# Optimization experiments

Measured on AMD Instinct MI355X. Metric: run time of the kernel, lower is better.

The kernel has to match this reference:

```python
import jax, jax.numpy as jnp
import numpy as np

EPS = 1e-5  # BatchNorm eps (torch default)

def _bn(x, mean, var, gamma, beta):
    # eval-mode BatchNorm over the trailing (heads, ch) axes
    return (x - mean) * (gamma / jnp.sqrt(var + EPS)) + beta

def setup_inputs() -> dict:
    key = jax.random.key(0)
    ks = jax.random.split(key, 8)
    B, C, W, H = 16, 256, 64, 64
    heads, k, u, m = 4, 16, 1, 23
    vv = 256
    kh, vh = k // heads, vv // heads
    x = jax.random.normal(ks[0], (B, C, W, H), dtype=jnp.float32)
    q_w = jax.random.normal(ks[1], (heads, kh, C), dtype=jnp.float32) * 0.05
    k_w = jax.random.normal(ks[2], (heads, kh * u, C), dtype=jnp.float32) * 0.05
    v_w = jax.random.normal(ks[3], (heads, vh * u, C), dtype=jnp.float32) * 0.05
    q_gamma = 0.5 + jax.random.uniform(ks[4], (heads, kh), dtype=jnp.float32)
    q_beta = jax.random.normal(ks[5], (heads, kh), dtype=jnp.float32) * 0.1
    q_mean = jnp.zeros((heads, kh), dtype=jnp.float32)
    q_var = jnp.ones((heads, kh), dtype=jnp.float32)
    k_gamma = 0.5 + jax.random.uniform(ks[6], (heads, kh * u), dtype=jnp.float32)
    k_beta = jax.random.normal(ks[7], (heads, kh * u), dtype=jnp.float32) * 0.1
    k_mean = jnp.zeros((heads, kh * u), dtype=jnp.float32)
    k_var = jnp.ones((heads, kh * u), dtype=jnp.float32)
    embedding = jax.random.normal(jax.random.fold_in(key, 99), (kh, heads, u, 1, m, m), dtype=jnp.float32) * 0.05
    return {"x": x, "q_w": q_w, "q_gamma": q_gamma, "q_beta": q_beta, "q_mean": q_mean,
            "q_var": q_var, "k_w": k_w, "k_gamma": k_gamma, "k_beta": k_beta,
            "k_mean": k_mean, "k_var": k_var, "v_w": v_w, "embedding": embedding}

def reference(x, q_w, q_gamma, q_beta, q_mean, q_var, k_w, k_gamma, k_beta, k_mean, k_var, v_w, embedding):
    B, C, W, H = x.shape
    heads, kh, _ = q_w.shape
    u = embedding.shape[2]
    m = embedding.shape[-1]
    vh = v_w.shape[1] // u
    pad = (m - 1) // 2

    # 1x1 conv projections (all heads stacked) -> channels-last
    q = jnp.einsum('bcxy,hkc->bxyhk', x, q_w)                      # [B,W,H,heads,kh]
    q = _bn(q, q_mean, q_var, q_gamma, q_beta)
    kk = jnp.einsum('bcxy,hkc->bxyhk', x, k_w)                     # [B,W,H,heads,kh*u]
    kk = _bn(kk, k_mean, k_var, k_gamma, k_beta)
    # softmax over all spatial positions, per (head, key-channel)
    sm = jax.nn.softmax(kk.reshape(B, W * H, heads, kh * u), axis=1)
    sm = sm.reshape(B, W, H, heads, kh, u)                          # [B,W,H,h,kh,u]
    v = jnp.einsum('bcxy,hvc->bxyhv', x, v_w).reshape(B, W, H, heads, vh, u)

    # content lambda: sum over all spatial positions
    lambda_c = jnp.einsum('bxyhku,bxyhvu->bhkv', sm, v)             # [B,h,kh,vh]
    y_c = jnp.einsum('bxyhk,bhkv->bxyhv', q, lambda_c)              # [B,W,H,h,vh]

    # positional lambda via grouped 2D conv (conv3d kernel depth is 1 -> 2D conv per vh slice)
    v_conv = v.transpose(0, 4, 3, 5, 1, 2).reshape(B * vh, heads * u, W, H)
    w = jnp.squeeze(embedding, axis=3).transpose(1, 0, 2, 3, 4).reshape(heads * kh, u, m, m)
    conv = jax.lax.conv_general_dilated(
        v_conv, w, window_strides=(1, 1), padding=[(pad, pad), (pad, pad)],
        dimension_numbers=('NCHW', 'OIHW', 'NCHW'), feature_group_count=heads)
    # [B*vh, heads*kh, W, H] -> sum over spatial (matches .sum(dim=[1,2]) in source)
    lambda_p = conv.reshape(B, vh, heads, kh, W, H).sum(axis=(4, 5))
    lambda_p = lambda_p.transpose(0, 2, 3, 1)                       # [B,h,kh,vh]
    y_p = jnp.einsum('bxyhk,bhkv->bxyhv', q, lambda_p)

    out = (y_c + y_p).reshape(B, W, H, heads * vh).transpose(0, 3, 1, 2)  # [B,vv,W,H]
    return out
```

## Files before the change

### kernel.cpp

```cpp
#include <hip/hip_runtime.h>
#include <math.h>

#define C_   256
#define WH   4096

typedef _Float16 f16x8 __attribute__((ext_vector_type(8)));
typedef float    f32x4 __attribute__((ext_vector_type(4)));


__global__ __launch_bounds__(512) void proj_kernel(
    const float* __restrict__ x,
    const float* __restrict__ qw, const float* __restrict__ kw,
    const float* __restrict__ qg, const float* __restrict__ qb,
    const float* __restrict__ qm, const float* __restrict__ qv,
    const float* __restrict__ kg, const float* __restrict__ kb,
    const float* __restrict__ km, const float* __restrict__ kv,
    const float* __restrict__ emb,
    float* __restrict__ qbn, float* __restrict__ kkbn,
    float* __restrict__ pstats, float* __restrict__ Wt)
{
    if (blockIdx.x >= 256) {
        int wb = blockIdx.x - 256;
        int hk = wb >> 2, quarter = wb & 3;
        int h = hk >> 2, k = hk & 3;
        const float* e = emb + (size_t)(k * 4 + h) * 529;
        __shared__ float colsum[23][64];
        for (int t2 = threadIdx.x; t2 < 23 * 64; t2 += 512) {
            int i = t2 / 64, q = t2 % 64;
            int jlo = max(0, q - 52), jhi = min(22, q + 11);
            float s = 0.f;
            for (int j = jlo; j <= jhi; ++j) s += e[i * 23 + j];
            colsum[i][q] = s;
        }
        __syncthreads();
        for (int tt = threadIdx.x; tt < 1024; tt += 512) {
            int t2 = quarter * 1024 + tt;
            int p = t2 >> 6, q = t2 & 63;
            int ilo = max(0, p - 52), ihi = min(22, p + 11);
            float s = 0.f;
            for (int i = ilo; i <= ihi; ++i) s += colsum[i][q];
            Wt[(size_t)hk * WH + t2] = s;
        }
        return;
    }

    int t = threadIdx.x;
    int b = blockIdx.x >> 4, chunk = blockIdx.x & 15;
    int lane = t & 63;
    int og = __builtin_amdgcn_readfirstlane(t >> 6);
    int isK = og >> 2;
    int o4 = (og & 3) * 4;
    int xy = chunk * 256 + lane * 4;

    const float* wsrc = isK ? kw : qw;
    const float* w0 = wsrc + (size_t)(o4 + 0) * 256;
    const float* w1 = wsrc + (size_t)(o4 + 1) * 256;
    const float* w2 = wsrc + (size_t)(o4 + 2) * 256;
    const float* w3 = wsrc + (size_t)(o4 + 3) * 256;

    float4 a0 = {0,0,0,0}, a1 = {0,0,0,0}, a2 = {0,0,0,0}, a3 = {0,0,0,0};
    const float* xb = x + (size_t)b * C_ * WH + xy;
#pragma unroll 8
    for (int c = 0; c < 256; ++c) {
        float4 xv = *(const float4*)(xb + (size_t)c * WH);
        float f0 = w0[c], f1 = w1[c], f2 = w2[c], f3 = w3[c];
        a0.x += xv.x*f0; a0.y += xv.y*f0; a0.z += xv.z*f0; a0.w += xv.w*f0;
        a1.x += xv.x*f1; a1.y += xv.y*f1; a1.z += xv.z*f1; a1.w += xv.w*f1;
        a2.x += xv.x*f2; a2.y += xv.y*f2; a2.z += xv.z*f2; a2.w += xv.w*f2;
        a3.x += xv.x*f3; a3.y += xv.y*f3; a3.z += xv.z*f3; a3.w += xv.w*f3;
    }
    float4 acc4[4] = {a0, a1, a2, a3};

    if (!isK) {
#pragma unroll
        for (int i = 0; i < 4; ++i) {
            int hk = o4 + i;
            float s  = qg[hk] * rsqrtf(qv[hk] + 1e-5f);
            float tq = qb[hk] - qm[hk] * s;
            float4 a = acc4[i], o;
            o.x = a.x * s + tq; o.y = a.y * s + tq;
            o.z = a.z * s + tq; o.w = a.w * s + tq;
            *(float4*)(qbn + ((size_t)b * 16 + hk) * WH + xy) = o;
        }
    } else {
#pragma unroll
        for (int i = 0; i < 4; ++i) {
            int hk = o4 + i;
            float s2 = kg[hk] * rsqrtf(kv[hk] + 1e-5f);
            float tk = kb[hk] - km[hk] * s2;
            float4 a = acc4[i], o;
            o.x = a.x * s2 + tk; o.y = a.y * s2 + tk;
            o.z = a.z * s2 + tk; o.w = a.w * s2 + tk;
            *(float4*)(kkbn + ((size_t)b * 16 + hk) * WH + xy) = o;
            float m = fmaxf(fmaxf(o.x, o.y), fmaxf(o.z, o.w));
#pragma unroll
            for (int off = 32; off; off >>= 1) m = fmaxf(m, __shfl_xor(m, off, 64));
            float e = __expf(o.x - m) + __expf(o.y - m) + __expf(o.z - m) + __expf(o.w - m);
#pragma unroll
            for (int off = 32; off; off >>= 1) e += __shfl_xor(e, off, 64);
            if (lane == 0) {
                float* ps = pstats + ((size_t)(b * 16 + hk) * 16 + chunk) * 2;
                ps[0] = m; ps[1] = e;
            }
        }
    }
}

__global__ __launch_bounds__(512) void ut_kernel(
    const float* __restrict__ x, const float* __restrict__ kkbn,
    const float* __restrict__ pstats, const float* __restrict__ Wt,
    float* __restrict__ Mpart)
{
    __shared__ _Float16 xls[256][72];
    __shared__ _Float16 wls[32][72];
    __shared__ float st[32];
    int t = threadIdx.x;
    int b = blockIdx.x >> 5, s5 = blockIdx.x & 31;
    int xys0 = s5 * 128;
    int lane = t & 63;
    int wid = __builtin_amdgcn_readfirstlane(t >> 6);
    int r16 = lane & 15, g = lane >> 4;
    int n0 = wid * 32;

    if (t < 16) {
        const float* ps = pstats + (size_t)(b * 16 + t) * 32;
        float M = ps[0];
#pragma unroll
        for (int ch = 1; ch < 16; ++ch) M = fmaxf(M, ps[ch * 2]);
        float S = 0.f;
#pragma unroll
        for (int ch = 0; ch < 16; ++ch) S += ps[ch * 2 + 1] * __expf(ps[ch * 2] - M);
        st[2 * t]     = M;
        st[2 * t + 1] = 1.f / S;
    }

    int sc = t >> 1, shalf = t & 1;
    int wr = t >> 3, wco = (t & 7) * 8;

    f32x4 acc00 = {0.f,0.f,0.f,0.f}, acc01 = {0.f,0.f,0.f,0.f};
    f32x4 acc10 = {0.f,0.f,0.f,0.f}, acc11 = {0.f,0.f,0.f,0.f};

    for (int ch = 0; ch < 2; ++ch) {
        int kbase = xys0 + ch * 64;
        __syncthreads();
        {
            const float* xp = x + ((size_t)b * C_ + sc) * WH + kbase + shalf * 32;
#pragma unroll
            for (int j = 0; j < 4; ++j) {
                float4 u  = *(const float4*)(xp + j * 8);
                float4 u2 = *(const float4*)(xp + j * 8 + 4);
                f16x8 o;
                o[0] = (_Float16)u.x;  o[1] = (_Float16)u.y;
                o[2] = (_Float16)u.z;  o[3] = (_Float16)u.w;
                o[4] = (_Float16)u2.x; o[5] = (_Float16)u2.y;
                o[6] = (_Float16)u2.z; o[7] = (_Float16)u2.w;
                *(f16x8*)&xls[sc][shalf * 32 + j * 8] = o;
            }
        }
        if (t < 256) {
            f16x8 o;
            if (wr < 16) {
                float wm   = st[2 * wr];
                float winv = st[2 * wr + 1];
                const float* src = kkbn + ((size_t)b * 16 + wr) * WH + kbase + wco;
                float4 u  = *(const float4*)(src);
                float4 u2 = *(const float4*)(src + 4);
                o[0] = (_Float16)(__expf(u.x  - wm) * winv);
                o[1] = (_Float16)(__expf(u.y  - wm) * winv);
                o[2] = (_Float16)(__expf(u.z  - wm) * winv);
                o[3] = (_Float16)(__expf(u.w  - wm) * winv);
                o[4] = (_Float16)(__expf(u2.x - wm) * winv);
                o[5] = (_Float16)(__expf(u2.y - wm) * winv);
                o[6] = (_Float16)(__expf(u2.z - wm) * winv);
                o[7] = (_Float16)(__expf(u2.w - wm) * winv);
            } else {
                const float* src = Wt + (size_t)(wr - 16) * WH + kbase + wco;
                float4 u  = *(const float4*)(src);
                float4 u2 = *(const float4*)(src + 4);
                o[0] = (_Float16)u.x;  o[1] = (_Float16)u.y;
                o[2] = (_Float16)u.z;  o[3] = (_Float16)u.w;
                o[4] = (_Float16)u2.x; o[5] = (_Float16)u2.y;
                o[6] = (_Float16)u2.z; o[7] = (_Float16)u2.w;
            }
            *(f16x8*)&wls[wr][wco] = o;
        }
        __syncthreads();
#pragma unroll
        for (int s = 0; s < 2; ++s) {
            int koff = s * 32 + g * 8;
            f16x8 A0 = *(const f16x8*)&wls[r16     ][koff];
            f16x8 A1 = *(const f16x8*)&wls[16 + r16][koff];
            f16x8 B0 = *(const f16x8*)&xls[n0 + r16     ][koff];
            f16x8 B1 = *(const f16x8*)&xls[n0 + 16 + r16][koff];
            acc00 = __builtin_amdgcn_mfma_f32_16x16x32_f16(A0, B0, acc00, 0, 0, 0);
            acc01 = __builtin_amdgcn_mfma_f32_16x16x32_f16(A0, B1, acc01, 0, 0, 0);
            acc10 = __builtin_amdgcn_mfma_f32_16x16x32_f16(A1, B0, acc10, 0, 0, 0);
            acc11 = __builtin_amdgcn_mfma_f32_16x16x32_f16(A1, B1, acc11, 0, 0, 0);
        }
    }

    float* mp = Mpart + (size_t)(b * 32 + s5) * 4096;
    int colA = n0 + r16, colB = n0 + 16 + r16;
    int row0 = g * 4;
#pragma unroll
    for (int rr = 0; rr < 4; ++rr) {
        mp[(row0 + rr) * 256 + colA] = acc00[rr] + acc10[rr];
        mp[(row0 + rr) * 256 + colB] = acc01[rr] + acc11[rr];
    }
}

__global__ __launch_bounds__(256) void out_kernel(
    const float* __restrict__ qbn, const float* __restrict__ Mpart,
    const float* __restrict__ vw, float* __restrict__ out)
{
    __shared__ float vls[64][260];
    __shared__ float msum[4][256];
    __shared__ float lam_s[4][64];
    int t = threadIdx.x;
    int b = blockIdx.x >> 4, s = blockIdx.x & 15;
    int h = s >> 2, qc = s & 3;

    {
        const float* vwh = vw + (size_t)h * 64 * 256;
#pragma unroll
        for (int i = 0; i < 16; ++i) {
            int e = t + i * 256;
            int vv = e >> 6, c4 = (e & 63) * 4;
            *(float4*)&vls[vv][c4] = *(const float4*)(vwh + (size_t)vv * 256 + c4);
        }
    }
    {
        const float* mp = Mpart + (size_t)b * 32 * 4096 + t;
#pragma unroll
        for (int rr = 0; rr < 4; ++rr) {
            const float* m2 = mp + (h * 4 + rr) * 256;
            float ssum = 0.f;
            for (int seg = 0; seg < 32; ++seg) ssum += m2[seg * 4096];
            msum[rr][t] = ssum;
        }
    }
    __syncthreads();
    {
        int rr = t >> 6, v = t & 63;
        float acc = 0.f;
#pragma unroll 8
        for (int c4 = 0; c4 < 64; ++c4) {
            float4 a = *(const float4*)&vls[v][c4 * 4];
            float4 m = *(const float4*)&msum[rr][c4 * 4];
            acc += a.x*m.x + a.y*m.y + a.z*m.z + a.w*m.w;
        }
        lam_s[rr][v] = acc;
    }
    __syncthreads();

    int xy = qc * 1024 + t * 4;
    float4 q0 = *(const float4*)(qbn + ((size_t)b * 16 + h * 4 + 0) * WH + xy);
    float4 q1 = *(const float4*)(qbn + ((size_t)b * 16 + h * 4 + 1) * WH + xy);
    float4 q2 = *(const float4*)(qbn + ((size_t)b * 16 + h * 4 + 2) * WH + xy);
    float4 q3 = *(const float4*)(qbn + ((size_t)b * 16 + h * 4 + 3) * WH + xy);
    float* ob = out + ((size_t)b * 256 + (size_t)h * 64) * WH + xy;
#pragma unroll 8
    for (int v = 0; v < 64; ++v) {
        float l0 = lam_s[0][v], l1 = lam_s[1][v], l2 = lam_s[2][v], l3 = lam_s[3][v];
        float4 o;
        o.x = q0.x*l0 + q1.x*l1 + q2.x*l2 + q3.x*l3;
        o.y = q0.y*l0 + q1.y*l1 + q2.y*l2 + q3.y*l3;
        o.z = q0.z*l0 + q1.z*l1 + q2.z*l2 + q3.z*l3;
        o.w = q0.w*l0 + q1.w*l1 + q2.w*l2 + q3.w*l3;
        *(float4*)(ob + (size_t)v * WH) = o;
    }
}

extern "C" void kernel_launch(void* const* d_in, const int* in_sizes, int n_in,
                              void* d_out, int out_size, void* d_ws, size_t ws_size,
                              hipStream_t stream)
{
    const float* x   = (const float*)d_in[0];
    const float* qw  = (const float*)d_in[1];
    const float* qg  = (const float*)d_in[2];
    const float* qb  = (const float*)d_in[3];
    const float* qm  = (const float*)d_in[4];
    const float* qv  = (const float*)d_in[5];
    const float* kw  = (const float*)d_in[6];
    const float* kg  = (const float*)d_in[7];
    const float* kb  = (const float*)d_in[8];
    const float* km  = (const float*)d_in[9];
    const float* kv  = (const float*)d_in[10];
    const float* vw  = (const float*)d_in[11];
    const float* emb = (const float*)d_in[12];

    float* ws     = (float*)d_ws;
    float* qbn    = ws;
    float* kkbn   = ws + 1048576;
    float* pstats = ws + 2097152;
    float* Wt     = ws + 2105344;
    float* Mpart  = ws + 2170880;
    float* out    = (float*)d_out;

    hipLaunchKernelGGL(proj_kernel,  dim3(320), dim3(512), 0, stream,
                       x, qw, kw, qg, qb, qm, qv, kg, kb, km, kv, emb,
                       qbn, kkbn, pstats, Wt);
    hipLaunchKernelGGL(ut_kernel,    dim3(512), dim3(512), 0, stream,
                       x, kkbn, pstats, Wt, Mpart);
    hipLaunchKernelGGL(out_kernel,   dim3(256), dim3(256), 0, stream,
                       qbn, Mpart, vw, out);
}
```

Baseline: 76.04 us.

## Fuse q/k projection and softmax into the MFMA reduction kernel

Merges the projection kernel into the kernel that reduces over spatial positions. Each block now computes q/k for its own 128-position window and writes exp(k) directly to LDS as fp16, so the kkbn round trip and the partial-stats pass go away. Softmax normalisation is deferred: per-row sums are gathered with atomicAdd and divided out in out_kernel. The unnormalized and positional partials are written separately, which doubles the Mpart traffic. Dropping the max subtraction risks exp overflow or fp16 overflow for large logits. The Wt precompute moves to its own small kernel, which also zeroes the sums.

```diff
diff --git a/kernel.cpp b/kernel.cpp
--- a/kernel.cpp
+++ b/kernel.cpp
@@ -5,143 +5,120 @@
 #define WH   4096
 
 typedef _Float16 f16x8 __attribute__((ext_vector_type(8)));
+typedef _Float16 f16x2 __attribute__((ext_vector_type(2)));
 typedef float    f32x4 __attribute__((ext_vector_type(4)));
 
 
-__global__ __launch_bounds__(512) void proj_kernel(
+__global__ __launch_bounds__(256) void wt_kernel(const float* __restrict__ emb,
+                                                 float* __restrict__ Wt,
+                                                 float* __restrict__ S)
+{
+    int wb = blockIdx.x;
+    if (threadIdx.x < 4) S[wb * 4 + threadIdx.x] = 0.f;
+    int hk = wb >> 2, quarter = wb & 3;
+    int h = hk >> 2, k = hk & 3;
+    const float* e = emb + (size_t)(k * 4 + h) * 529;
+    __shared__ float colsum[23][64];
+    for (int t = threadIdx.x; t < 23 * 64; t += 256) {
+        int i = t / 64, q = t % 64;
+        int jlo = max(0, q - 52), jhi = min(22, q + 11);
+        float s = 0.f;
+        for (int j = jlo; j <= jhi; ++j) s += e[i * 23 + j];
+        colsum[i][q] = s;
+    }
+    __syncthreads();
+    for (int tt = threadIdx.x; tt < 1024; tt += 256) {
+        int t = quarter * 1024 + tt;
+        int p = t >> 6, q = t & 63;
+        int ilo = max(0, p - 52), ihi = min(22, p + 11);
+        float s = 0.f;
+        for (int i = ilo; i <= ihi; ++i) s += colsum[i][q];
+        Wt[(size_t)hk * WH + t] = s;
+    }
+}
+
+__global__ __launch_bounds__(512) void main_kernel(
     const float* __restrict__ x,
     const float* __restrict__ qw, const float* __restrict__ kw,
     const float* __restrict__ qg, const float* __restrict__ qb,
     const float* __restrict__ qm, const float* __restrict__ qv,
     const float* __restrict__ kg, const float* __restrict__ kb,
     const float* __restrict__ km, const float* __restrict__ kv,
-    const float* __restrict__ emb,
-    float* __restrict__ qbn, float* __restrict__ kkbn,
-    float* __restrict__ pstats, float* __restrict__ Wt)
-{
-    if (blockIdx.x >= 256) {
-        int wb = blockIdx.x - 256;
-        int hk = wb >> 2, quarter = wb & 3;
-        int h = hk >> 2, k = hk & 3;
-        const float* e = emb + (size_t)(k * 4 + h) * 529;
-        __shared__ float colsum[23][64];
-        for (int t2 = threadIdx.x; t2 < 23 * 64; t2 += 512) {
-            int i = t2 / 64, q = t2 % 64;
-            int jlo = max(0, q - 52), jhi = min(22, q + 11);
-            float s = 0.f;
-            for (int j = jlo; j <= jhi; ++j) s += e[i * 23 + j];
-            colsum[i][q] = s;
-        }
-        __syncthreads();
-        for (int tt = threadIdx.x; tt < 1024; tt += 512) {
-            int t2 = quarter * 1024 + tt;
-            int p = t2 >> 6, q = t2 & 63;
-            int ilo = max(0, p - 52), ihi = min(22, p + 11);
-            float s = 0.f;
-            for (int i = ilo; i <= ihi; ++i) s += colsum[i][q];
-            Wt[(size_t)hk * WH + t2] = s;
-        }
-        return;
-    }
-
-    int t = threadIdx.x;
-    int b = blockIdx.x >> 4, chunk = blockIdx.x & 15;
-    int lane = t & 63;
-    int og = __builtin_amdgcn_readfirstlane(t >> 6);
-    int isK = og >> 2;
-    int o4 = (og & 3) * 4;
-    int xy = chunk * 256 + lane * 4;
-
-    const float* wsrc = isK ? kw : qw;
-    const float* w0 = wsrc + (size_t)(o4 + 0) * 256;
-    const float* w1 = wsrc + (size_t)(o4 + 1) * 256;
-    const float* w2 = wsrc + (size_t)(o4 + 2) * 256;
-    const float* w3 = wsrc + (size_t)(o4 + 3) * 256;
-
-    float4 a0 = {0,0,0,0}, a1 = {0,0,0,0}, a2 = {0,0,0,0}, a3 = {0,0,0,0};
-    const float* xb = x + (size_t)b * C_ * WH + xy;
+    const float* __restrict__ Wt,
+    float* __restrict__ qbn, float* __restrict__ S, float* __restrict__ Mpart)
+{
+    __shared__ _Float16 xls[256][72];
+    __shared__ _Float16 ebuf[16][136];
+    __shared__ _Float16 wtbuf[16][136];
+    int t = threadIdx.x, lane = t & 63;
+    int w = __builtin_amdgcn_readfirstlane(t >> 6);
+    int b = blockIdx.x >> 5, s5 = blockIdx.x & 31;
+    int win = s5 * 128;
+
+    if (t < 256) {
+        int r = t >> 4, xo = (t & 15) * 8;
+        const float* src = Wt + (size_t)r * WH + win + xo;
+        float4 u = *(const float4*)src, u2 = *(const float4*)(src + 4);
+        _Float16* d = &wtbuf[r][xo];
+        d[0]=(_Float16)u.x;  d[1]=(_Float16)u.y;  d[2]=(_Float16)u.z;  d[3]=(_Float16)u.w;
+        d[4]=(_Float16)u2.x; d[5]=(_Float16)u2.y; d[6]=(_Float16)u2.z; d[7]=(_Float16)u2.w;
+    }
+
+    {
+        int isK = w >> 2;
+        int r0 = (w & 3) * 4;
+        const float* wsrc = isK ? kw : qw;
+        const float* w0 = wsrc + (size_t)(r0 + 0) * 256;
+        const float* w1 = wsrc + (size_t)(r0 + 1) * 256;
+        const float* w2 = wsrc + (size_t)(r0 + 2) * 256;
+        const float* w3 = wsrc + (size_t)(r0 + 3) * 256;
+        float2 a0 = {0,0}, a1 = {0,0}, a2 = {0,0}, a3 = {0,0};
+        const float* xb = x + (size_t)b * C_ * WH + win + lane * 2;
 #pragma unroll 8
-    for (int c = 0; c < 256; ++c) {
-        float4 xv = *(const float4*)(xb + (size_t)c * WH);
-        float f0 = w0[c], f1 = w1[c], f2 = w2[c], f3 = w3[c];
-        a0.x += xv.x*f0; a0.y += xv.y*f0; a0.z += xv.z*f0; a0.w += xv.w*f0;
-        a1.x += xv.x*f1; a1.y += xv.y*f1; a1.z += xv.z*f1; a1.w += xv.w*f1;
-        a2.x += xv.x*f2; a2.y += xv.y*f2; a2.z += xv.z*f2; a2.w += xv.w*f2;
-        a3.x += xv.x*f3; a3.y += xv.y*f3; a3.z += xv.z*f3; a3.w += xv.w*f3;
-    }
-    float4 acc4[4] = {a0, a1, a2, a3};
-
-    if (!isK) {
-#pragma unroll
-        for (int i = 0; i < 4; ++i) {
-            int hk = o4 + i;
-            float s  = qg[hk] * rsqrtf(qv[hk] + 1e-5f);
-            float tq = qb[hk] - qm[hk] * s;
-            float4 a = acc4[i], o;
-            o.x = a.x * s + tq; o.y = a.y * s + tq;
-            o.z = a.z * s + tq; o.w = a.w * s + tq;
-            *(float4*)(qbn + ((size_t)b * 16 + hk) * WH + xy) = o;
-        }
-    } else {
-#pragma unroll
-        for (int i = 0; i < 4; ++i) {
-            int hk = o4 + i;
-            float s2 = kg[hk] * rsqrtf(kv[hk] + 1e-5f);
-            float tk = kb[hk] - km[hk] * s2;
-            float4 a = acc4[i], o;
-            o.x = a.x * s2 + tk; o.y = a.y * s2 + tk;
-            o.z = a.z * s2 + tk; o.w = a.w * s2 + tk;
-            *(float4*)(kkbn + ((size_t)b * 16 + hk) * WH + xy) = o;
-            float m = fmaxf(fmaxf(o.x, o.y), fmaxf(o.z, o.w));
-#pragma unroll
-            for (int off = 32; off; off >>= 1) m = fmaxf(m, __shfl_xor(m, off, 64));
-            float e = __expf(o.x - m) + __expf(o.y - m) + __expf(o.z - m) + __expf(o.w - m);
-#pragma unroll
-            for (int off = 32; off; off >>= 1) e += __shfl_xor(e, off, 64);
-            if (lane == 0) {
-                float* ps = pstats + ((size_t)(b * 16 + hk) * 16 + chunk) * 2;
-                ps[0] = m; ps[1] = e;
-            }
-        }
-    }
-}
-
-__global__ __launch_bounds__(512) void ut_kernel(
-    const float* __restrict__ x, const float* __restrict__ kkbn,
-    const float* __restrict__ pstats, const float* __restrict__ Wt,
-    float* __restrict__ Mpart)
-{
-    __shared__ _Float16 xls[256][72];
-    __shared__ _Float16 wls[32][72];
-    __shared__ float st[32];
-    int t = threadIdx.x;
-    int b = blockIdx.x >> 5, s5 = blockIdx.x & 31;
-    int xys0 = s5 * 128;
-    int lane = t & 63;
-    int wid = __builtin_amdgcn_readfirstlane(t >> 6);
+        for (int c = 0; c < 256; ++c) {
+            float2 xv = *(const float2*)(xb + (size_t)c * WH);
+            float f0 = w0[c], f1 = w1[c], f2 = w2[c], f3 = w3[c];
+            a0.x += xv.x*f0; a0.y += xv.y*f0;
+            a1.x += xv.x*f1; a1.y += xv.y*f1;
+            a2.x += xv.x*f2; a2.y += xv.y*f2;
+            a3.x += xv.x*f3; a3.y += xv.y*f3;
+        }
+        float2 acc2[4] = {a0, a1, a2, a3};
+        if (!isK) {
+#pragma unroll
+            for (int i = 0; i < 4; ++i) {
+                int hk = r0 + i;
+                float s  = qg[hk] * rsqrtf(qv[hk] + 1e-5f);
+                float tq = qb[hk] - qm[hk] * s;
+                float2 o; o.x = acc2[i].x * s + tq; o.y = acc2[i].y * s + tq;
+                *(float2*)(qbn + ((size_t)b * 16 + hk) * WH + win + lane * 2) = o;
+            }
+        } else {
+#pragma unroll
+            for (int i = 0; i < 4; ++i) {
+                int hk = r0 + i;
+                float s2 = kg[hk] * rsqrtf(kv[hk] + 1e-5f);
+                float tk = kb[hk] - km[hk] * s2;
+                float e0 = __expf(acc2[i].x * s2 + tk);
+                float e1 = __expf(acc2[i].y * s2 + tk);
+                f16x2 p; p[0] = (_Float16)e0; p[1] = (_Float16)e1;
+                *(f16x2*)&ebuf[hk][lane * 2] = p;
+                float ssum = e0 + e1;
+#pragma unroll
+                for (int off = 32; off; off >>= 1) ssum += __shfl_xor(ssum, off, 64);
+                if (lane == 0) atomicAdd(&S[b * 16 + hk], ssum);
+            }
+        }
+    }
+
     int r16 = lane & 15, g = lane >> 4;
-    int n0 = wid * 32;
-
-    if (t < 16) {
-        const float* ps = pstats + (size_t)(b * 16 + t) * 32;
-        float M = ps[0];
-#pragma unroll
-        for (int ch = 1; ch < 16; ++ch) M = fmaxf(M, ps[ch * 2]);
-        float S = 0.f;
-#pragma unroll
-        for (int ch = 0; ch < 16; ++ch) S += ps[ch * 2 + 1] * __expf(ps[ch * 2] - M);
-        st[2 * t]     = M;
-        st[2 * t + 1] = 1.f / S;
-    }
-
+    int n0 = w * 32;
     int sc = t >> 1, shalf = t & 1;
-    int wr = t >> 3, wco = (t & 7) * 8;
-
     f32x4 acc00 = {0.f,0.f,0.f,0.f}, acc01 = {0.f,0.f,0.f,0.f};
     f32x4 acc10 = {0.f,0.f,0.f,0.f}, acc11 = {0.f,0.f,0.f,0.f};
 
     for (int ch = 0; ch < 2; ++ch) {
-        int kbase = xys0 + ch * 64;
+        int kbase = win + ch * 64;
         __syncthreads();
         {
             const float* xp = x + ((size_t)b * C_ + sc) * WH + kbase + shalf * 32;
@@ -157,39 +134,13 @@
                 *(f16x8*)&xls[sc][shalf * 32 + j * 8] = o;
             }
         }
-        if (t < 256) {
-            f16x8 o;
-            if (wr < 16) {
-                float wm   = st[2 * wr];
-                float winv = st[2 * wr + 1];
-                const float* src = kkbn + ((size_t)b * 16 + wr) * WH + kbase + wco;
-                float4 u  = *(const float4*)(src);
-                float4 u2 = *(const float4*)(src + 4);
-                o[0] = (_Float16)(__expf(u.x  - wm) * winv);
-                o[1] = (_Float16)(__expf(u.y  - wm) * winv);
-                o[2] = (_Float16)(__expf(u.z  - wm) * winv);
-                o[3] = (_Float16)(__expf(u.w  - wm) * winv);
-                o[4] = (_Float16)(__expf(u2.x - wm) * winv);
-                o[5] = (_Float16)(__expf(u2.y - wm) * winv);
-                o[6] = (_Float16)(__expf(u2.z - wm) * winv);
-                o[7] = (_Float16)(__expf(u2.w - wm) * winv);
-            } else {
-                const float* src = Wt + (size_t)(wr - 16) * WH + kbase + wco;
-                float4 u  = *(const float4*)(src);
-                float4 u2 = *(const float4*)(src + 4);
-                o[0] = (_Float16)u.x;  o[1] = (_Float16)u.y;
-                o[2] = (_Float16)u.z;  o[3] = (_Float16)u.w;
-                o[4] = (_Float16)u2.x; o[5] = (_Float16)u2.y;
-                o[6] = (_Float16)u2.z; o[7] = (_Float16)u2.w;
-            }
-            *(f16x8*)&wls[wr][wco] = o;
-        }
         __syncthreads();
 #pragma unroll
         for (int s = 0; s < 2; ++s) {
-            int koff = s * 32 + g * 8;
-            f16x8 A0 = *(const f16x8*)&wls[r16     ][koff];
-            f16x8 A1 = *(const f16x8*)&wls[16 + r16][koff];
+            int koff  = s * 32 + g * 8;
+            int ko128 = ch * 64 + koff;
+            f16x8 A0 = *(const f16x8*)&ebuf [r16][ko128];
+            f16x8 A1 = *(const f16x8*)&wtbuf[r16][ko128];
             f16x8 B0 = *(const f16x8*)&xls[n0 + r16     ][koff];
             f16x8 B1 = *(const f16x8*)&xls[n0 + 16 + r16][koff];
             acc00 = __builtin_amdgcn_mfma_f32_16x16x32_f16(A0, B0, acc00, 0, 0, 0);
@@ -199,27 +150,32 @@
         }
     }
 
-    float* mp = Mpart + (size_t)(b * 32 + s5) * 4096;
+    float* mp = Mpart + (size_t)(b * 32 + s5) * 8192;
     int colA = n0 + r16, colB = n0 + 16 + r16;
     int row0 = g * 4;
 #pragma unroll
     for (int rr = 0; rr < 4; ++rr) {
-        mp[(row0 + rr) * 256 + colA] = acc00[rr] + acc10[rr];
-        mp[(row0 + rr) * 256 + colB] = acc01[rr] + acc11[rr];
+        mp[(row0 + rr) * 256 + colA]        = acc00[rr];
+        mp[(row0 + rr) * 256 + colB]        = acc01[rr];
+        mp[4096 + (row0 + rr) * 256 + colA] = acc10[rr];
+        mp[4096 + (row0 + rr) * 256 + colB] = acc11[rr];
     }
 }
 
 __global__ __launch_bounds__(256) void out_kernel(
     const float* __restrict__ qbn, const float* __restrict__ Mpart,
-    const float* __restrict__ vw, float* __restrict__ out)
+    const float* __restrict__ S, const float* __restrict__ vw,
+    float* __restrict__ out)
 {
     __shared__ float vls[64][260];
     __shared__ float msum[4][256];
     __shared__ float lam_s[4][64];
+    __shared__ float sinv[4];
     int t = threadIdx.x;
     int b = blockIdx.x >> 4, s = blockIdx.x & 15;
     int h = s >> 2, qc = s & 3;
 
+    if (t < 4) sinv[t] = 1.f / S[b * 16 + h * 4 + t];
     {
         const float* vwh = vw + (size_t)h * 64 * 256;
 #pragma unroll
@@ -229,14 +185,18 @@
             *(float4*)&vls[vv][c4] = *(const float4*)(vwh + (size_t)vv * 256 + c4);
         }
     }
-    {
-        const float* mp = Mpart + (size_t)b * 32 * 4096 + t;
+    __syncthreads();
+    {
+        const float* mp = Mpart + (size_t)b * 32 * 8192 + t;
 #pragma unroll
         for (int rr = 0; rr < 4; ++rr) {
-            const float* m2 = mp + (h * 4 + rr) * 256;
-            float ssum = 0.f;
-            for (int seg = 0; seg < 32; ++seg) ssum += m2[seg * 4096];
-            msum[rr][t] = ssum;
+            const float* mu = mp + (h * 4 + rr) * 256;
+            float su = 0.f, st2 = 0.f;
+            for (int s5 = 0; s5 < 32; ++s5) {
+                su  += mu[s5 * 8192];
+                st2 += mu[s5 * 8192 + 4096];
+            }
+            msum[rr][t] = su * sinv[rr] + st2;
         }
     }
     __syncthreads();
@@ -289,19 +249,17 @@
     const float* vw  = (const float*)d_in[11];
     const float* emb = (const float*)d_in[12];
 
-    float* ws     = (float*)d_ws;
-    float* qbn    = ws;
-    float* kkbn   = ws + 1048576;
-    float* pstats = ws + 2097152;
-    float* Wt     = ws + 2105344;
-    float* Mpart  = ws + 2170880;
-    float* out    = (float*)d_out;
-
-    hipLaunchKernelGGL(proj_kernel,  dim3(320), dim3(512), 0, stream,
-                       x, qw, kw, qg, qb, qm, qv, kg, kb, km, kv, emb,
-                       qbn, kkbn, pstats, Wt);
-    hipLaunchKernelGGL(ut_kernel,    dim3(512), dim3(512), 0, stream,
-                       x, kkbn, pstats, Wt, Mpart);
-    hipLaunchKernelGGL(out_kernel,   dim3(256), dim3(256), 0, stream,
-                       qbn, Mpart, vw, out);
-}
+    float* ws    = (float*)d_ws;
+    float* qbn   = ws;
+    float* Sv    = ws + 1048576;
+    float* Wt    = ws + 1048832;
+    float* Mpart = ws + 1114368;
+    float* out   = (float*)d_out;
+
+    hipLaunchKernelGGL(wt_kernel,   dim3(64),  dim3(256), 0, stream, emb, Wt, Sv);
+    hipLaunchKernelGGL(main_kernel, dim3(512), dim3(512), 0, stream,
+                       x, qw, kw, qg, qb, qm, qv, kg, kb, km, kv, Wt,
+                       qbn, Sv, Mpart);
+    hipLaunchKernelGGL(out_kernel,  dim3(256), dim3(256), 0, stream,
+                       qbn, Mpart, Sv, vw, out);
+}
```

Result: slower. 121.5 us (+59.8%).
